# Kernel tuning notes

Hardware: AMD Instinct MI355X
Metric: run time of the kernel (lower is better)

## Reference

```python
import jax, jax.numpy as jnp
import numpy as np

N_NODES = 100000
N_EDGES = 3200000
NFEAT, NHID, NCLASS = 512, 256, 64


def spmm(rows, cols, vals, x):
    # out[i] = sum_{e: rows[e]==i} vals[e] * x[cols[e]]
    msgs = vals[:, None] * x[cols]  # [E, F]
    return jax.ops.segment_sum(msgs, rows, num_segments=N_NODES)


def setup_inputs() -> dict:
    key = jax.random.key(0)
    ks = jax.random.split(key, 12)
    x = jax.random.normal(ks[0], (N_NODES, NFEAT), dtype=jnp.float32)
    adj_rows = jax.random.randint(ks[1], (N_EDGES,), 0, N_NODES, dtype=jnp.int32)
    adj_cols = jax.random.randint(ks[2], (N_EDGES,), 0, N_NODES, dtype=jnp.int32)
    adj_vals = jax.random.uniform(ks[3], (N_EDGES,), dtype=jnp.float32)
    # xavier-uniform style init for linear weights
    def xavier(k, fan_in, fan_out):
        a = np.sqrt(6.0 / (fan_in + fan_out)).astype(np.float32)
        return jax.random.uniform(k, (fan_in, fan_out), minval=-a, maxval=a, dtype=jnp.float32)
    W1 = xavier(ks[4], NFEAT, NHID)
    b1 = jnp.zeros((NHID,), dtype=jnp.float32)
    W2 = xavier(ks[5], NHID, NCLASS)
    b2 = jnp.zeros((NCLASS,), dtype=jnp.float32)
    Wres = xavier(ks[6], NHID, NCLASS)
    bres = jnp.zeros((NCLASS,), dtype=jnp.float32)
    return {"x": x, "adj_rows": adj_rows, "adj_cols": adj_cols, "adj_vals": adj_vals,
            "W1": W1, "b1": b1, "W2": W2, "b2": b2, "Wres": Wres, "bres": bres}


def reference(x, adj_rows, adj_cols, adj_vals, W1, b1, W2, b2, Wres, bres):
    # layer 1: spmm -> linear (res_con True but last_hidden is None -> no residual)
    h = spmm(adj_rows, adj_cols, adj_vals, x)          # [N, NFEAT]
    h = h @ W1 + b1                                    # [N, NHID]
    last_hidden = h
    # dropout in eval mode: identity
    # layer 2: spmm -> linear -> relu + res(last_hidden) since NHID != NCLASS
    o = spmm(adj_rows, adj_cols, adj_vals, h)          # [N, NHID]
    o = o @ W2 + b2                                    # [N, NCLASS]
    o = jax.nn.relu(o) + (last_hidden @ Wres + bres)   # [N, NCLASS]
    return o
```

## Files before the change

kernel.cpp:

```cpp
#include <hip/hip_runtime.h>

#define N_NODES 100000
#define N_EDGES 3200000
#define NFEAT 512
#define NHID 256
#define NCLASS 64
#define FCAT 128

#define RPB 32
#define NB 3125
#define CHUNK 8192
#define NCH 391

#define SC1 131072.0f
#define ISC1 (1.0f / 131072.0f)
#define SC2 16384.0f
#define ISC2 (1.0f / 16384.0f)
#define SCR 1048576.0f
#define ISCR (1.0f / 1048576.0f)
#define MAGICF 12582912.0f
#define MAGICI 0x4B400000

typedef __attribute__((ext_vector_type(8))) short short8;
typedef __attribute__((ext_vector_type(4))) float f32x4;

static __device__ __forceinline__ unsigned short f2bf(float f) {
    unsigned u = __float_as_uint(f);
    unsigned r = (u + 0x7FFF + ((u >> 16) & 1)) >> 16;
    return (unsigned short)r;
}
static __device__ __forceinline__ float bf2f(unsigned s) {
    return __uint_as_float(s << 16);
}
static __device__ __forceinline__ int f2fix(float vs, float a) {
    return __float_as_int(fmaf(vs, a, MAGICF)) - MAGICI;
}
static __device__ __forceinline__ short8 cvt8(float4 x, float4 y) {
    short8 r;
    r[0] = (short)f2bf(x.x); r[1] = (short)f2bf(x.y);
    r[2] = (short)f2bf(x.z); r[3] = (short)f2bf(x.w);
    r[4] = (short)f2bf(y.x); r[5] = (short)f2bf(y.y);
    r[6] = (short)f2bf(y.z); r[7] = (short)f2bf(y.w);
    return r;
}
__device__ __forceinline__ void gload_lds16(const unsigned short* g, unsigned short* l) {
    __builtin_amdgcn_global_load_lds(
        (const __attribute__((address_space(1))) unsigned int*)g,
        (__attribute__((address_space(3))) unsigned int*)l, 16, 0, 0);
}

__global__ void k_prep_wcat(const float* __restrict__ W1, const float* __restrict__ W2,
                            const float* __restrict__ Wres, unsigned short* __restrict__ WT) {
    int k = blockIdx.x;
    int j = threadIdx.x;
    const float* wb = (j < NCLASS) ? W2 : Wres;
    int jj = j & (NCLASS - 1);
    const float* w1row = W1 + (size_t)k * NHID;
    float acc = 0.f;
    for (int m = 0; m < NHID; ++m)
        acc += w1row[m] * wb[(size_t)m * NCLASS + jj];
    WT[(size_t)j * NFEAT + k] = f2bf(acc);
}

__global__ void k_prep_c(const float* __restrict__ b1, const float* __restrict__ W2,
                         const float* __restrict__ Wres, const float* __restrict__ bres,
                         float* __restrict__ c2, float* __restrict__ cr) {
    int j = threadIdx.x;
    const float* wb = (j < NCLASS) ? W2 : Wres;
    int jj = j & (NCLASS - 1);
    float acc = 0.f;
    for (int m = 0; m < NHID; ++m)
        acc += b1[m] * wb[(size_t)m * NCLASS + jj];
    if (j < NCLASS) c2[jj] = acc;
    else            cr[jj] = acc + bres[jj];
}

#define GBK 64
__global__ __launch_bounds__(256) void k_gemm_a(const float* __restrict__ X,
                                                const unsigned short* __restrict__ WT,
                                                unsigned* __restrict__ A2) {
    __shared__ __align__(16) unsigned short Bs[2][FCAT * GBK];
    int tid = threadIdx.x;
    int lane = tid & 63, w = tid >> 6;
    int lr = lane & 15, ls = lane >> 4;
    int row = blockIdx.x * 64 + w * 16 + lr;
    if (row >= N_NODES) row = N_NODES - 1;
    const float* pA = X + (size_t)row * NFEAT;

#define STAGE(buf, k0)                                                         \
    {                                                                          \
        _Pragma("unroll")                                                      \
        for (int q = 0; q < 4; ++q) {                                          \
            int sidx = q * 256 + tid;                                          \
            int n = sidx >> 3, c8 = sidx & 7;                                  \
            const unsigned short* src =                                        \
                WT + (size_t)n * NFEAT + (k0) + ((c8 ^ (n & 7)) << 3);         \
            unsigned short* dst = &Bs[buf][(size_t)(q * 256 + w * 64) * 8];    \
            gload_lds16(src, dst);                                             \
        }                                                                      \
    }

    f32x4 acc[8] = {};
    STAGE(0, 0);
    __syncthreads();
    int cur = 0;

#pragma unroll
    for (int t = 0; t < 8; ++t) {
        const int k0 = t * GBK;
        float4 a00 = *(const float4*)(pA + k0 + ls * 8);
        float4 a01 = *(const float4*)(pA + k0 + ls * 8 + 4);
        float4 a10 = *(const float4*)(pA + k0 + 32 + ls * 8);
        float4 a11 = *(const float4*)(pA + k0 + 32 + ls * 8 + 4);
        if (t < 7) STAGE(cur ^ 1, k0 + GBK);

        short8 af0 = cvt8(a00, a01);
        short8 af1 = cvt8(a10, a11);
        const unsigned short* bb = &Bs[cur][0];
#pragma unroll
        for (int nf = 0; nf < 8; ++nf) {
            int n = nf * 16 + lr;
            int p0 = ls ^ (n & 7);
            int p1 = (4 + ls) ^ (n & 7);
            short8 b0 = *(const short8*)(bb + (size_t)n * 64 + p0 * 8);
            short8 b1 = *(const short8*)(bb + (size_t)n * 64 + p1 * 8);
            acc[nf] = __builtin_amdgcn_mfma_f32_16x16x32_bf16(af0, b0, acc[nf], 0, 0, 0);
            acc[nf] = __builtin_amdgcn_mfma_f32_16x16x32_bf16(af1, b1, acc[nf], 0, 0, 0);
        }
        __syncthreads();
        cur ^= 1;
    }
#undef STAGE

#pragma unroll
    for (int j = 0; j < 4; ++j) {
        int gr = blockIdx.x * 64 + w * 16 + ls * 4 + j;
        if (gr < N_NODES) {
#pragma unroll
            for (int nf = 0; nf < 4; ++nf) {
                unsigned lo = f2bf(acc[nf][j]);
                unsigned hi = f2bf(acc[nf + 4][j]);
                A2[(size_t)gr * 64 + nf * 16 + lr] = lo | (hi << 16);
            }
        }
    }
}

__global__ __launch_bounds__(256) void k_hist_bkt(const int* __restrict__ rows,
                                                  int* __restrict__ HT) {
    __shared__ int h[NB];
    int c = blockIdx.x;
    for (int i = threadIdx.x; i < NB; i += 256) h[i] = 0;
    __syncthreads();
    int e0 = c * CHUNK;
    int eend = e0 + CHUNK; if (eend > N_EDGES) eend = N_EDGES;
    int i = e0 + threadIdx.x;
    for (; i + 7 * 256 < eend; i += 8 * 256) {
        int r[8];
#pragma unroll
        for (int u = 0; u < 8; ++u) r[u] = rows[i + u * 256];
#pragma unroll
        for (int u = 0; u < 8; ++u) atomicAdd(&h[r[u] >> 5], 1);
    }
    for (; i < eend; i += 256)
        atomicAdd(&h[rows[i] >> 5], 1);
    __syncthreads();
    for (int k = threadIdx.x; k < NB; k += 256)
        HT[(size_t)k * NCH + c] = h[k];
}

__global__ void k_scan_chunks(const int* __restrict__ HT, int* __restrict__ OFS,
                              int* __restrict__ T) {
    int b = blockIdx.x;
    int lane = threadIdx.x;
    const int* hb = HT + (size_t)b * NCH;
    int run = 0;
    for (int c0 = 0; c0 < NCH; c0 += 64) {
        int idx = c0 + lane;
        int v = (idx < NCH) ? hb[idx] : 0;
        int inc = v;
#pragma unroll
        for (int d = 1; d < 64; d <<= 1) {
            int t = __shfl_up(inc, d);
            if (lane >= d) inc += t;
        }
        if (idx < NCH) OFS[(size_t)idx * NB + b] = run + inc - v;
        run += __shfl(inc, 63);
    }
    if (lane == 0) T[b] = run;
}

__global__ void k_scan_base(const int* __restrict__ T, int* __restrict__ base) {
    int lane = threadIdx.x;
    int run = 0;
    for (int c0 = 0; c0 < NB; c0 += 64) {
        int idx = c0 + lane;
        int v = (idx < NB) ? T[idx] : 0;
        int inc = v;
#pragma unroll
        for (int d = 1; d < 64; d <<= 1) {
            int t = __shfl_up(inc, d);
            if (lane >= d) inc += t;
        }
        if (idx < NB) base[idx] = run + inc - v;
        run += __shfl(inc, 63);
    }
    if (lane == 0) base[NB] = run;
}

__global__ __launch_bounds__(256) void k_partition(const int* __restrict__ rows,
                                                   const int* __restrict__ cols,
                                                   const float* __restrict__ vals,
                                                   const int* __restrict__ OFS,
                                                   const int* __restrict__ base,
                                                   int2* __restrict__ stage) {
    __shared__ int cur[NB];
    int c = blockIdx.x;
    for (int i = threadIdx.x; i < NB; i += 256)
        cur[i] = base[i] + OFS[(size_t)c * NB + i];
    __syncthreads();
    int e0 = c * CHUNK;
    int eend = e0 + CHUNK; if (eend > N_EDGES) eend = N_EDGES;
    int i = e0 + threadIdx.x;
    for (; i + 7 * 256 < eend; i += 8 * 256) {
        int r[8], cc[8]; float v[8];
#pragma unroll
        for (int u = 0; u < 8; ++u) r[u] = rows[i + u * 256];
#pragma unroll
        for (int u = 0; u < 8; ++u) cc[u] = cols[i + u * 256];
#pragma unroll
        for (int u = 0; u < 8; ++u) v[u] = vals[i + u * 256];
        int p[8];
#pragma unroll
        for (int u = 0; u < 8; ++u) p[u] = atomicAdd(&cur[r[u] >> 5], 1);
#pragma unroll
        for (int u = 0; u < 8; ++u)
            stage[p[u]] = make_int2(((r[u] & 31) << 17) | cc[u], __float_as_int(v[u]));
    }
    for (; i < eend; i += 256) {
        int r = rows[i];
        int p = atomicAdd(&cur[r >> 5], 1);
        stage[p] = make_int2(((r & 31) << 17) | cols[i], __float_as_int(vals[i]));
    }
}

__global__ __launch_bounds__(256) void k_spmm1(const unsigned* __restrict__ A2,
                                               const int* __restrict__ base,
                                               const int2* __restrict__ stage,
                                               unsigned short* __restrict__ S1a,
                                               float* __restrict__ S1r) {
    __shared__ int acc[RPB][FCAT];
    int b = blockIdx.x, tid = threadIdx.x;
    int wv = tid >> 6, lane = tid & 63;
    int4* az = (int4*)&acc[0][0];
    for (int i = tid; i < RPB * FCAT / 4; i += 256) az[i] = make_int4(0, 0, 0, 0);
    __syncthreads();

    int s = base[b], e = base[b + 1];
    int per = (e - s + 3) >> 2;
    int ws = s + wv * per;
    int we = ws + per; if (we > e) we = e;
    int t = ws;
    for (; t + 16 <= we; t += 16) {
        int2 cv[16];
#pragma unroll
        for (int u = 0; u < 16; ++u) cv[u] = stage[t + u];
        unsigned p[16];
#pragma unroll
        for (int u = 0; u < 16; ++u)
            p[u] = A2[(size_t)(cv[u].x & 0x1FFFF) * 64 + lane];
#pragma unroll
        for (int u = 0; u < 16; ++u) {
            float vs = __int_as_float(cv[u].y) * SC1;
            int rl = ((unsigned)cv[u].x) >> 17;
            atomicAdd(&acc[rl][lane],      f2fix(vs, bf2f(p[u] & 0xffffu)));
            atomicAdd(&acc[rl][lane + 64], f2fix(vs, bf2f(p[u] >> 16)));
        }
    }
    for (; t < we; ++t) {
        int2 cv = stage[t];
        unsigned p = A2[(size_t)(cv.x & 0x1FFFF) * 64 + lane];
        float vs = __int_as_float(cv.y) * SC1;
        int rl = ((unsigned)cv.x) >> 17;
        atomicAdd(&acc[rl][lane],      f2fix(vs, bf2f(p & 0xffffu)));
        atomicAdd(&acc[rl][lane + 64], f2fix(vs, bf2f(p >> 16)));
    }
    __syncthreads();

#pragma unroll
    for (int rr = 0; rr < 8; ++rr) {
        int r = wv * 8 + rr;
        int node = b * RPB + r;
        float c0 = (float)acc[r][lane] * ISC1;
        float c1 = (float)acc[r][lane + 64] * ISC1;
        S1a[(size_t)node * 64 + (lane & 31) * 2 + (lane >> 5)] = f2bf(c0);
        S1r[(size_t)node * 64 + lane] = c1;
    }
}

__global__ __launch_bounds__(256) void k_spmm2_out(const unsigned* __restrict__ S1aP,
                                                   const float* __restrict__ S1r,
                                                   const int* __restrict__ base,
                                                   const int2* __restrict__ stage,
                                                   const float* __restrict__ c2,
                                                   const float* __restrict__ cr,
                                                   const float* __restrict__ b2,
                                                   float* __restrict__ out) {
    __shared__ int acc[RPB][NCLASS];
    __shared__ int rs[RPB];
    int b = blockIdx.x, tid = threadIdx.x;
    int wv = tid >> 6, lane = tid & 63;
    int h = lane >> 5, l5 = lane & 31;
    int4* az = (int4*)&acc[0][0];
    for (int i = tid; i < RPB * NCLASS / 4; i += 256) az[i] = make_int4(0, 0, 0, 0);
    if (tid < RPB) rs[tid] = 0;
    __syncthreads();

    int s = base[b], e = base[b + 1];
    int per = (e - s + 3) >> 2;
    int ws = s + wv * per;
    int we = ws + per; if (we > e) we = e;
    int t = ws;
    for (; t + 16 <= we; t += 16) {
        int2 cv[8];
#pragma unroll
        for (int u = 0; u < 8; ++u) cv[u] = stage[t + u * 2 + h];
        unsigned p[8];
#pragma unroll
        for (int u = 0; u < 8; ++u)
            p[u] = S1aP[(size_t)(cv[u].x & 0x1FFFF) * 32 + l5];
#pragma unroll
        for (int u = 0; u < 8; ++u) {
            float v = __int_as_float(cv[u].y);
            float vs = v * SC2;
            int rl = ((unsigned)cv[u].x) >> 17;
            atomicAdd(&acc[rl][l5],      f2fix(vs, bf2f(p[u] & 0xffffu)));
            atomicAdd(&acc[rl][l5 + 32], f2fix(vs, bf2f(p[u] >> 16)));
            if (l5 == 0) atomicAdd(&rs[rl], f2fix(v, SCR));
        }
    }
    for (; t < we; t += 2) {
        int idx = t + h;
        bool act = idx < we;
        int2 cv = stage[act ? idx : t];
        unsigned p = S1aP[(size_t)(cv.x & 0x1FFFF) * 32 + l5];
        float v = __int_as_float(cv.y);
        float vs = v * SC2;
        int rl = ((unsigned)cv.x) >> 17;
        if (act) {
            atomicAdd(&acc[rl][l5],      f2fix(vs, bf2f(p & 0xffffu)));
            atomicAdd(&acc[rl][l5 + 32], f2fix(vs, bf2f(p >> 16)));
            if (l5 == 0) atomicAdd(&rs[rl], f2fix(v, SCR));
        }
    }
    __syncthreads();

#pragma unroll
    for (int rr = 0; rr < 8; ++rr) {
        int r = wv * 8 + rr;
        int node = b * RPB + r;
        float facc = (float)acc[r][lane] * ISC2;
        float rsum = (float)rs[r] * ISCR;
        float o = facc + rsum * c2[lane] + b2[lane];
        float res = S1r[(size_t)node * 64 + lane] + cr[lane];
        out[(size_t)node * 64 + lane] = fmaxf(o, 0.f) + res;
    }
}

extern "C" void kernel_launch(void* const* d_in, const int* in_sizes, int n_in,
                              void* d_out, int out_size, void* d_ws, size_t ws_size,
                              hipStream_t stream) {
    const float* x        = (const float*)d_in[0];
    const int*   adj_rows = (const int*)d_in[1];
    const int*   adj_cols = (const int*)d_in[2];
    const float* adj_vals = (const float*)d_in[3];
    const float* W1       = (const float*)d_in[4];
    const float* b1       = (const float*)d_in[5];
    const float* W2       = (const float*)d_in[6];
    const float* b2       = (const float*)d_in[7];
    const float* Wres     = (const float*)d_in[8];
    const float* bres     = (const float*)d_in[9];
    float* out = (float*)d_out;

    char* ws = (char*)d_ws;
    size_t off = 0;
    auto alloc = [&](size_t bytes) {
        size_t o = off;
        off += (bytes + 511) & ~511ULL;
        return o;
    };

    unsigned short* WT  = (unsigned short*)(ws + alloc((size_t)NFEAT * FCAT * 2));
    float* c2           = (float*)(ws + alloc(NCLASS * 4));
    float* cr           = (float*)(ws + alloc(NCLASS * 4));
    int2* stage         = (int2*)(ws + alloc((size_t)N_EDGES * 8));
    unsigned* A2        = (unsigned*)(ws + alloc((size_t)N_NODES * 64 * 4));
    unsigned* S1a       = (unsigned*)(ws + alloc((size_t)N_NODES * 32 * 4));
    char* s1r_region    = ws + alloc((size_t)N_NODES * 64 * 4);
    float* S1r          = (float*)s1r_region;
    int*   HT           = (int*)s1r_region;
    int*   OFS          = (int*)(s1r_region + (((size_t)NB * NCH * 4 + 511) & ~511ULL));
    int*   T            = (int*)(ws + alloc((size_t)NB * 4));
    int*   base         = (int*)(ws + alloc((size_t)(NB + 1) * 4));
    (void)ws_size; (void)in_sizes; (void)n_in; (void)out_size;

    k_prep_wcat<<<NFEAT, FCAT, 0, stream>>>(W1, W2, Wres, WT);
    k_prep_c<<<1, FCAT, 0, stream>>>(b1, W2, Wres, bres, c2, cr);

    k_hist_bkt<<<NCH, 256, 0, stream>>>(adj_rows, HT);
    k_scan_chunks<<<NB, 64, 0, stream>>>(HT, OFS, T);
    k_scan_base<<<1, 64, 0, stream>>>(T, base);
    k_partition<<<NCH, 256, 0, stream>>>(adj_rows, adj_cols, adj_vals, OFS, base, stage);

    k_gemm_a<<<(N_NODES + 63) / 64, 256, 0, stream>>>(x, WT, A2);

    k_spmm1<<<NB, 256, 0, stream>>>(A2, base, stage, (unsigned short*)S1a, S1r);

    k_spmm2_out<<<NB, 256, 0, stream>>>(S1a, S1r, base, stage, c2, cr, b2, out);
}
```

Measured before the change: 387.4 us.

## Replace bf16/float fixed-point accumulation with int16 Q10 integer arithmetic in SpMM

Stores the projected features and intermediate SpMM1 results as clamped 16-bit fixed-point integers (Q10 / Q-scaled) instead of bf16, and quantizes edge values to Q10 integers in the staged edge list. The gather and accumulate then use integer multiply (mul24) and shifts rather than bf16 decode plus float FMA with the magic-number conversion, and the column index is pre-shifted so the gather address needs only a mask-and-or. This removes per-edge conversion ALU work but clamps activations to about ±16 and coarsens the precision of edge weights and features, which risks accuracy loss.

```diff
diff --git a/kernel.cpp b/kernel.cpp
--- a/kernel.cpp
+++ b/kernel.cpp
@@ -12,14 +12,9 @@
 #define CHUNK 8192
 #define NCH 391
 
-#define SC1 131072.0f
-#define ISC1 (1.0f / 131072.0f)
-#define SC2 16384.0f
-#define ISC2 (1.0f / 16384.0f)
-#define SCR 1048576.0f
-#define ISCR (1.0f / 1048576.0f)
-#define MAGICF 12582912.0f
-#define MAGICI 0x4B400000
+#define ISC20 (1.0f / 1048576.0f)
+#define ISC14 (1.0f / 16384.0f)
+#define ISC10 (1.0f / 1024.0f)
 
 typedef __attribute__((ext_vector_type(8))) short short8;
 typedef __attribute__((ext_vector_type(4))) float f32x4;
@@ -28,12 +23,6 @@
     unsigned u = __float_as_uint(f);
     unsigned r = (u + 0x7FFF + ((u >> 16) & 1)) >> 16;
     return (unsigned short)r;
-}
-static __device__ __forceinline__ float bf2f(unsigned s) {
-    return __uint_as_float(s << 16);
-}
-static __device__ __forceinline__ int f2fix(float vs, float a) {
-    return __float_as_int(fmaf(vs, a, MAGICF)) - MAGICI;
 }
 static __device__ __forceinline__ short8 cvt8(float4 x, float4 y) {
     short8 r;
@@ -47,6 +36,9 @@
     __builtin_amdgcn_global_load_lds(
         (const __attribute__((address_space(1))) unsigned int*)g,
         (__attribute__((address_space(3))) unsigned int*)l, 16, 0, 0);
+}
+static __device__ __forceinline__ int f2q10(float a) {
+    return __float2int_rn(fminf(fmaxf(a, -15.98f), 15.98f) * 1024.f);
 }
 
 __global__ void k_prep_wcat(const float* __restrict__ W1, const float* __restrict__ W2,
@@ -138,9 +130,10 @@
         if (gr < N_NODES) {
 #pragma unroll
             for (int nf = 0; nf < 4; ++nf) {
-                unsigned lo = f2bf(acc[nf][j]);
-                unsigned hi = f2bf(acc[nf + 4][j]);
-                A2[(size_t)gr * 64 + nf * 16 + lr] = lo | (hi << 16);
+                int il = f2q10(acc[nf][j]);
+                int ih = f2q10(acc[nf + 4][j]);
+                A2[(size_t)gr * 64 + nf * 16 + lr] =
+                    ((unsigned)il & 0xffffu) | ((unsigned)ih << 16);
             }
         }
     }
@@ -235,12 +228,15 @@
         for (int u = 0; u < 8; ++u) p[u] = atomicAdd(&cur[r[u] >> 5], 1);
 #pragma unroll
         for (int u = 0; u < 8; ++u)
-            stage[p[u]] = make_int2(((r[u] & 31) << 17) | cc[u], __float_as_int(v[u]));
+            stage[p[u]] = make_int2((int)(((unsigned)(r[u] & 31) << 27) |
+                                          ((unsigned)cc[u] << 8)),
+                                    __float2int_rn(v[u] * 1024.f));
     }
     for (; i < eend; i += 256) {
         int r = rows[i];
         int p = atomicAdd(&cur[r >> 5], 1);
-        stage[p] = make_int2(((r & 31) << 17) | cols[i], __float_as_int(vals[i]));
+        stage[p] = make_int2((int)(((unsigned)(r & 31) << 27) | ((unsigned)cols[i] << 8)),
+                             __float2int_rn(vals[i] * 1024.f));
     }
 }
 
@@ -252,9 +248,12 @@
     __shared__ int acc[RPB][FCAT];
     int b = blockIdx.x, tid = threadIdx.x;
     int wv = tid >> 6, lane = tid & 63;
+    unsigned lane4 = (unsigned)lane << 2;
     int4* az = (int4*)&acc[0][0];
     for (int i = tid; i < RPB * FCAT / 4; i += 256) az[i] = make_int4(0, 0, 0, 0);
     __syncthreads();
+
+    const char* A2b = (const char*)A2;
 
     int s = base[b], e = base[b + 1];
     int per = (e - s + 3) >> 2;
@@ -268,22 +267,26 @@
         unsigned p[16];
 #pragma unroll
         for (int u = 0; u < 16; ++u)
-            p[u] = A2[(size_t)(cv[u].x & 0x1FFFF) * 64 + lane];
+            p[u] = *(const unsigned*)(A2b + ((((unsigned)cv[u].x) & 0x07FFFF00u) | lane4));
 #pragma unroll
         for (int u = 0; u < 16; ++u) {
-            float vs = __int_as_float(cv[u].y) * SC1;
-            int rl = ((unsigned)cv[u].x) >> 17;
-            atomicAdd(&acc[rl][lane],      f2fix(vs, bf2f(p[u] & 0xffffu)));
-            atomicAdd(&acc[rl][lane + 64], f2fix(vs, bf2f(p[u] >> 16)));
+            int v10 = cv[u].y;
+            int alo = (int)(short)(p[u] & 0xffffu);
+            int ahi = (int)p[u] >> 16;
+            int rl = (int)(((unsigned)cv[u].x) >> 27);
+            atomicAdd(&acc[rl][lane],      __mul24(alo, v10));
+            atomicAdd(&acc[rl][lane + 64], __mul24(ahi, v10));
         }
     }
     for (; t < we; ++t) {
         int2 cv = stage[t];
-        unsigned p = A2[(size_t)(cv.x & 0x1FFFF) * 64 + lane];
-        float vs = __int_as_float(cv.y) * SC1;
-        int rl = ((unsigned)cv.x) >> 17;
-        atomicAdd(&acc[rl][lane],      f2fix(vs, bf2f(p & 0xffffu)));
-        atomicAdd(&acc[rl][lane + 64], f2fix(vs, bf2f(p >> 16)));
+        unsigned p = *(const unsigned*)(A2b + ((((unsigned)cv.x) & 0x07FFFF00u) | lane4));
+        int v10 = cv.y;
+        int alo = (int)(short)(p & 0xffffu);
+        int ahi = (int)p >> 16;
+        int rl = (int)(((unsigned)cv.x) >> 27);
+        atomicAdd(&acc[rl][lane],      __mul24(alo, v10));
+        atomicAdd(&acc[rl][lane + 64], __mul24(ahi, v10));
     }
     __syncthreads();
 
@@ -291,10 +294,10 @@
     for (int rr = 0; rr < 8; ++rr) {
         int r = wv * 8 + rr;
         int node = b * RPB + r;
-        float c0 = (float)acc[r][lane] * ISC1;
-        float c1 = (float)acc[r][lane + 64] * ISC1;
-        S1a[(size_t)node * 64 + (lane & 31) * 2 + (lane >> 5)] = f2bf(c0);
-        S1r[(size_t)node * 64 + lane] = c1;
+        int sf = (acc[r][lane] + 2048) >> 12;
+        sf = max(-32760, min(32760, sf));
+        S1a[(size_t)node * 64 + (lane & 31) * 2 + (lane >> 5)] = (unsigned short)sf;
+        S1r[(size_t)node * 64 + lane] = (float)acc[r][lane + 64] * ISC20;
     }
 }
 
@@ -311,10 +314,13 @@
     int b = blockIdx.x, tid = threadIdx.x;
     int wv = tid >> 6, lane = tid & 63;
     int h = lane >> 5, l5 = lane & 31;
+    unsigned l54 = (unsigned)l5 << 2;
     int4* az = (int4*)&acc[0][0];
     for (int i = tid; i < RPB * NCLASS / 4; i += 256) az[i] = make_int4(0, 0, 0, 0);
     if (tid < RPB) rs[tid] = 0;
     __syncthreads();
+
+    const char* Sb = (const char*)S1aP;
 
     int s = base[b], e = base[b + 1];
     int per = (e - s + 3) >> 2;
@@ -328,29 +334,31 @@
         unsigned p[8];
 #pragma unroll
         for (int u = 0; u < 8; ++u)
-            p[u] = S1aP[(size_t)(cv[u].x & 0x1FFFF) * 32 + l5];
+            p[u] = *(const unsigned*)(Sb + (((((unsigned)cv[u].x) & 0x07FFFF00u) >> 1) | l54));
 #pragma unroll
         for (int u = 0; u < 8; ++u) {
-            float v = __int_as_float(cv[u].y);
-            float vs = v * SC2;
-            int rl = ((unsigned)cv[u].x) >> 17;
-            atomicAdd(&acc[rl][l5],      f2fix(vs, bf2f(p[u] & 0xffffu)));
-            atomicAdd(&acc[rl][l5 + 32], f2fix(vs, bf2f(p[u] >> 16)));
-            if (l5 == 0) atomicAdd(&rs[rl], f2fix(v, SCR));
+            int v10 = cv[u].y;
+            int slo = (int)(short)(p[u] & 0xffffu);
+            int shi = (int)p[u] >> 16;
+            int rl = (int)(((unsigned)cv[u].x) >> 27);
+            atomicAdd(&acc[rl][l5],      (__mul24(slo, v10) + 8) >> 4);
+            atomicAdd(&acc[rl][l5 + 32], (__mul24(shi, v10) + 8) >> 4);
+            if (l5 == 0) atomicAdd(&rs[rl], v10);
         }
     }
     for (; t < we; t += 2) {
         int idx = t + h;
         bool act = idx < we;
         int2 cv = stage[act ? idx : t];
-        unsigned p = S1aP[(size_t)(cv.x & 0x1FFFF) * 32 + l5];
-        float v = __int_as_float(cv.y);
-        float vs = v * SC2;
-        int rl = ((unsigned)cv.x) >> 17;
+        unsigned p = *(const unsigned*)(Sb + (((((unsigned)cv.x) & 0x07FFFF00u) >> 1) | l54));
+        int v10 = cv.y;
+        int slo = (int)(short)(p & 0xffffu);
+        int shi = (int)p >> 16;
+        int rl = (int)(((unsigned)cv.x) >> 27);
         if (act) {
-            atomicAdd(&acc[rl][l5],      f2fix(vs, bf2f(p & 0xffffu)));
-            atomicAdd(&acc[rl][l5 + 32], f2fix(vs, bf2f(p >> 16)));
-            if (l5 == 0) atomicAdd(&rs[rl], f2fix(v, SCR));
+            atomicAdd(&acc[rl][l5],      (__mul24(slo, v10) + 8) >> 4);
+            atomicAdd(&acc[rl][l5 + 32], (__mul24(shi, v10) + 8) >> 4);
+            if (l5 == 0) atomicAdd(&rs[rl], v10);
         }
     }
     __syncthreads();
@@ -359,8 +367,8 @@
     for (int rr = 0; rr < 8; ++rr) {
         int r = wv * 8 + rr;
         int node = b * RPB + r;
-        float facc = (float)acc[r][lane] * ISC2;
-        float rsum = (float)rs[r] * ISCR;
+        float facc = (float)acc[r][lane] * ISC14;
+        float rsum = (float)rs[r] * ISC10;
         float o = facc + rsum * c2[lane] + b2[lane];
         float res = S1r[(size_t)node * 64 + lane] + cr[lane];
         out[(size_t)node * 64 + lane] = fmaxf(o, 0.f) + res;
```

After: 396.2 us. +2.3%, slower.
